# Optimization experiments

Measured on AMD Instinct MI355X. Metric: run time of the kernel, lower is better.

The kernel has to match this reference:

```python
import jax, jax.numpy as jnp
import numpy as np

H = 16      # num_heads
D = 64      # head_dim
HS = H * D  # hidden_size
B = 8
S = 1024


def setup_inputs() -> dict:
    key = jax.random.key(0)
    ks = jax.random.split(key, 12)
    scale = 1.0 / np.sqrt(HS)
    inp = {
        "v": jax.random.normal(ks[0], (B, S, HS), jnp.float32),
        "k": jax.random.normal(ks[1], (B, S, HS), jnp.float32),
        "q": jax.random.normal(ks[2], (B, S, HS), jnp.float32),
        "mask": jax.random.randint(ks[3], (B, 1, 1, S), 0, 2).astype(bool),
        "Wq": jax.random.normal(ks[4], (HS, HS), jnp.float32) * scale,
        "bq": jnp.zeros((HS,), jnp.float32),
        "Wk": jax.random.normal(ks[5], (HS, HS), jnp.float32) * scale,
        "bk": jnp.zeros((HS,), jnp.float32),
        "Wv": jax.random.normal(ks[6], (HS, HS), jnp.float32) * scale,
        "bv": jnp.zeros((HS,), jnp.float32),
        "Wo": jax.random.normal(ks[7], (HS, HS), jnp.float32) * scale,
        "bo": jnp.zeros((HS,), jnp.float32),
    }
    return inp


def _split_heads(x):
    b, s, _ = x.shape
    return x.reshape(b, s, H, D).transpose(0, 2, 1, 3)  # [B,H,S,D]


def reference(v, k, q, mask, Wq, bq, Wk, bk, Wv, bv, Wo, bo):
    # torch Linear: y = x @ W.T + b
    qh = _split_heads(q @ Wq.T + bq)
    kh = _split_heads(k @ Wk.T + bk)
    vh = _split_heads(v @ Wv.T + bv)
    scores = jnp.einsum("bhqd,bhkd->bhqk", qh, kh) / jnp.sqrt(jnp.float32(D))
    scores = jnp.where(mask, jnp.float32(-1e9), scores)
    att = jax.nn.softmax(scores, axis=-1)
    out = jnp.einsum("bhqk,bhkd->bhqd", att, vh)  # [B,H,S,D]
    out = out.transpose(0, 2, 1, 3).reshape(v.shape[0], -1, HS)
    return out @ Wo.T + bo
```

## Files before the change

kernel.cpp:

```cpp
#include <hip/hip_runtime.h>
#include <hip/hip_bf16.h>

#define HH   16
#define DD   64
#define HSZ  1024
#define BB   8
#define SS   1024
#define NTOK (BB*SS)
#define LOG2E 1.4426950408889634f
#define NCVTB 2048

typedef __attribute__((ext_vector_type(8))) short bf16x8;
typedef __attribute__((ext_vector_type(4))) float f32x4;
typedef unsigned short u16;
typedef __attribute__((ext_vector_type(4))) unsigned short u16x4;

__device__ __forceinline__ u16 bfc(float x) {
    __hip_bfloat16 h = __float2bfloat16(x);
    return *(u16*)&h;
}

__device__ __forceinline__ float exp2fast(float x) {
    return __builtin_amdgcn_exp2f(x);
}

__device__ __forceinline__ void gload16(const u16* g, u16* l) {
    __builtin_amdgcn_global_load_lds(
        (const __attribute__((address_space(1))) void*)g,
        (__attribute__((address_space(3))) void*)l, 16, 0, 0);
}

__device__ __forceinline__ void mask_scan_body(const void* mask,
                                               int* __restrict__ rmap,
                                               int* __restrict__ Larr, int b) {
    const int tid = threadIdx.x;
    const unsigned char* mball = (const unsigned char*)mask;

    __shared__ int fmt_s;
    __shared__ int wtot[4];
    __shared__ int Ls;
    if (tid == 0) fmt_s = 0;
    __syncthreads();
    int nz = 0;
    for (int i = tid; i < BB * SS; i += 256)
        if ((i & 3) && mball[i]) nz = 1;
    if (nz) fmt_s = 1;
    __syncthreads();
    const int fmt = fmt_s;

    const int base = tid * 4;
    int v[4];
#pragma unroll
    for (int e = 0; e < 4; ++e) {
        int val = fmt ? (int)mball[(size_t)b * SS + base + e]
                      : ((const int*)mask)[(size_t)b * SS + base + e];
        v[e] = (val == 0) ? 1 : 0;
    }
    int ts = v[0] + v[1] + v[2] + v[3];

    const int lane = tid & 63, wv = tid >> 6;
    int incl = ts;
#pragma unroll
    for (int d = 1; d < 64; d <<= 1) {
        int t = __shfl_up(incl, d);
        if (lane >= d) incl += t;
    }
    if (lane == 63) wtot[wv] = incl;
    __syncthreads();
    int woff = 0;
    for (int w = 0; w < wv; ++w) woff += wtot[w];
    int run = woff + incl - ts;
#pragma unroll
    for (int e = 0; e < 4; ++e) {
        if (v[e]) rmap[(size_t)b * SS + run] = base + e;
        run += v[e];
    }
    __syncthreads();
    if (tid == 0) {
        Ls = wtot[0] + wtot[1] + wtot[2] + wtot[3];
        Larr[b] = Ls;
    }
    __syncthreads();
    for (int j = Ls + tid; j < SS; j += 256) rmap[(size_t)b * SS + j] = 0;
}

__global__ __launch_bounds__(256) void cvt_scan_kernel(
        const float* __restrict__ q,  u16* __restrict__ dq,
        const float* __restrict__ k,  u16* __restrict__ dk,
        const float* __restrict__ v,  u16* __restrict__ dv,
        const float* __restrict__ w0, u16* __restrict__ dw0,
        const float* __restrict__ w1, u16* __restrict__ dw1,
        const float* __restrict__ w2, u16* __restrict__ dw2,
        const float* __restrict__ w3, u16* __restrict__ dw3,
        const void* mask, int* __restrict__ rmap, int* __restrict__ Larr) {
    if (blockIdx.x >= NCVTB) {
        mask_scan_body(mask, rmap, Larr, blockIdx.x - NCVTB);
        return;
    }
    const int NX = NTOK * HSZ / 8;
    const int NW = HSZ * HSZ / 8;
    const int ntot = 3 * NX + 4 * NW;
    int i = blockIdx.x * blockDim.x + threadIdx.x;
    const int stride = NCVTB * 256;
    for (; i < ntot; i += stride) {
        const float* s; u16* d; int j = i;
        if      (j < NX)            { s = q;  d = dq;  }
        else if ((j -= NX) < NX)    { s = k;  d = dk;  }
        else if ((j -= NX) < NX)    { s = v;  d = dv;  }
        else if ((j -= NX) < NW)    { s = w0; d = dw0; }
        else if ((j -= NW) < NW)    { s = w1; d = dw1; }
        else if ((j -= NW) < NW)    { s = w2; d = dw2; }
        else    { j -= NW;            s = w3; d = dw3; }
        f32x4 a = *(const f32x4*)&s[(size_t)j * 8];
        f32x4 b = *(const f32x4*)&s[(size_t)j * 8 + 4];
        union { bf16x8 v8; u16 u[8]; } t;
#pragma unroll
        for (int e = 0; e < 4; ++e) { t.u[e] = bfc(a[e]); t.u[4 + e] = bfc(b[e]); }
        *(bf16x8*)&d[(size_t)j * 8] = t.v8;
    }
}

template<int MODE>
__device__ __forceinline__ void proj_body(const u16* __restrict__ X,
                                          const u16* __restrict__ W,
                                          const float* __restrict__ bias,
                                          const int* __restrict__ rmap,
                                          const int* __restrict__ Larr,
                                          void* __restrict__ Yv,
                                          u16* Xs, u16* Ws) {
    const int bm = blockIdx.x;
    const int bn = blockIdx.y;
    const int tid  = threadIdx.x;
    const int wave = tid >> 6;
    const int lane = tid & 63;
    const int l15  = lane & 15;
    const int g    = lane >> 4;
    const int wr   = wave >> 1;
    const int wc   = wave & 1;

    const int b_   = bm >> 3;
    const int row0 = (bm & 7) * 128;
    if constexpr (MODE == 1 || MODE == 2) {
        const int L = Larr[b_];
        const int Lpad = ((L + 127) >> 7) << 7;
        if (row0 >= Lpad) return;
    }

    f32x4 acc[4][4] = {};

    int srow[4], scol[4], xr[4];
#pragma unroll
    for (int i = 0; i < 4; ++i) {
        const int slot = wave * 256 + i * 64 + lane;
        const int r = slot >> 3, s = slot & 7;
        srow[i] = r;
        scol[i] = (s ^ (r & 7)) * 8;
        if constexpr (MODE == 1 || MODE == 2)
            xr[i] = (b_ << 10) + rmap[(size_t)b_ * SS + row0 + r];
        else
            xr[i] = bm * 128 + r;
    }

    for (int k0 = 0; k0 < HSZ; k0 += 64) {
#pragma unroll
        for (int i = 0; i < 4; ++i) {
            gload16(&X[(size_t)xr[i] * HSZ + k0 + scol[i]], &Xs[(wave * 4 + i) * 512]);
            gload16(&W[(size_t)(bn * 128 + srow[i]) * HSZ + k0 + scol[i]],
                    &Ws[(wave * 4 + i) * 512]);
        }
        __syncthreads();

#pragma unroll
        for (int kk = 0; kk < 2; ++kk) {
            const int cw = ((kk * 4 + g) ^ (l15 & 7)) * 8;
            bf16x8 a[4], bb[4];
#pragma unroll
            for (int m = 0; m < 4; ++m)
                a[m] = *(const bf16x8*)&Xs[(size_t)(wr * 64 + m * 16 + l15) * 64 + cw];
#pragma unroll
            for (int n = 0; n < 4; ++n)
                bb[n] = *(const bf16x8*)&Ws[(size_t)(wc * 64 + n * 16 + l15) * 64 + cw];
#pragma unroll
            for (int m = 0; m < 4; ++m)
#pragma unroll
                for (int n = 0; n < 4; ++n)
                    acc[m][n] = __builtin_amdgcn_mfma_f32_16x16x32_bf16(a[m], bb[n], acc[m][n], 0, 0, 0);
        }
        __syncthreads();
    }

#pragma unroll
    for (int m = 0; m < 4; ++m) {
#pragma unroll
        for (int n = 0; n < 4; ++n) {
            const int o = bn * 128 + wc * 64 + n * 16 + l15;
            const float bvv = bias[o];
            const int h_ = o >> 6, d = o & 63;
#pragma unroll
            for (int r = 0; r < 4; ++r) {
                const int lrow = wr * 64 + m * 16 + g * 4 + r;
                float y = acc[m][n][r] + bvv;
                if constexpr (MODE == 0) {
                    const int nrow = bm * 128 + lrow;
                    int bb_ = nrow >> 10, s = nrow & 1023;
                    ((u16*)Yv)[(((size_t)bb_ * HH + h_) * SS + s) * DD + d] = bfc(y * (0.125f * LOG2E));
                } else if constexpr (MODE == 1) {
                    ((u16*)Yv)[(((size_t)b_ * HH + h_) * SS + row0 + lrow) * DD + d] = bfc(y);
                } else if constexpr (MODE == 2) {
                    ((u16*)Yv)[(((size_t)b_ * HH + h_) * DD + d) * SS + row0 + lrow] = bfc(y);
                } else {
                    const int nrow = bm * 128 + lrow;
                    ((float*)Yv)[(size_t)nrow * HSZ + o] = y;
                }
            }
        }
    }
}

__global__ __launch_bounds__(256) void proj_qkv_kernel(
        const u16* __restrict__ qbf, const u16* __restrict__ wqb,
        const float* __restrict__ bq, u16* __restrict__ Qh,
        const u16* __restrict__ kbf, const u16* __restrict__ wkb,
        const float* __restrict__ bk, u16* __restrict__ Kh,
        const u16* __restrict__ vbf, const u16* __restrict__ wvb,
        const float* __restrict__ bv, u16* __restrict__ Vt,
        const int* __restrict__ rmap, const int* __restrict__ Larr) {
    __shared__ u16 Xs[128 * 64];
    __shared__ u16 Ws[128 * 64];
    if (blockIdx.z == 0)      proj_body<0>(qbf, wqb, bq, rmap, Larr, Qh, Xs, Ws);
    else if (blockIdx.z == 1) proj_body<1>(kbf, wkb, bk, rmap, Larr, Kh, Xs, Ws);
    else                      proj_body<2>(vbf, wvb, bv, rmap, Larr, Vt, Xs, Ws);
}

__global__ __launch_bounds__(256) void proj_o_kernel(
        const u16* __restrict__ X, const u16* __restrict__ W,
        const float* __restrict__ bias, const int* __restrict__ rmap,
        const int* __restrict__ Larr, float* __restrict__ out) {
    __shared__ u16 Xs[128 * 64];
    __shared__ u16 Ws[128 * 64];
    proj_body<3>(X, W, bias, rmap, Larr, out, Xs, Ws);
}

__global__ __launch_bounds__(256, 2) void attn_kernel(const u16* __restrict__ Qh,
                                                      const u16* __restrict__ Kh,
                                                      const u16* __restrict__ Vt,
                                                      const int* __restrict__ Larr,
                                                      u16* __restrict__ ctx) {
    const int qt = blockIdx.x;
    const int h  = blockIdx.y;
    const int b  = blockIdx.z;
    const int bh = b * HH + h;

    const int tid  = threadIdx.x;
    const int wave = tid >> 6;
    const int lane = tid & 63;
    const int l15  = lane & 15;
    const int g    = lane >> 4;
    const int qw0  = qt * 256 + wave * 64;

    __shared__ u16 Pw[4][2][16][72];

    const u16* Qb = Qh + ((size_t)bh * SS + qw0) * DD;
    const u16* Kb = Kh + (size_t)bh * SS * DD;
    const u16* Vb = Vt + (size_t)bh * DD * SS;

    const int L = Larr[b];
    const int npairs = (L + 127) >> 7;

    bf16x8 qf[4][2];
#pragma unroll
    for (int qq = 0; qq < 4; ++qq)
#pragma unroll
        for (int hh = 0; hh < 2; ++hh)
            qf[qq][hh] = *(const bf16x8*)&Qb[(size_t)(qq * 16 + l15) * DD + hh * 32 + g * 8];

    f32x4 o[4][4] = {};
    float mrun[4] = { -3e38f, -3e38f, -3e38f, -3e38f };
    float lrun[4] = { 0.0f, 0.0f, 0.0f, 0.0f };

    auto loadK = [&](bf16x8 (&kbX)[8], int c0) {
#pragma unroll
        for (int kt = 0; kt < 4; ++kt)
#pragma unroll
            for (int hh = 0; hh < 2; ++hh)
                kbX[kt * 2 + hh] =
                    *(const bf16x8*)&Kb[(size_t)(c0 + kt * 16 + l15) * DD + hh * 32 + g * 8];
    };
    auto loadV = [&](bf16x8 (&vbX)[8], int c0) {
#pragma unroll
        for (int dt = 0; dt < 4; ++dt)
#pragma unroll
            for (int kh = 0; kh < 2; ++kh)
                vbX[dt * 2 + kh] =
                    *(const bf16x8*)&Vb[(size_t)(dt * 16 + l15) * SS + c0 + kh * 32 + g * 8];
    };

    auto process = [&](const bf16x8 (&kbX)[8], const bf16x8 (&vbX)[8], int c0) {
#pragma unroll
        for (int qq = 0; qq < 4; ++qq) {
            f32x4 s[4];
#pragma unroll
            for (int kt = 0; kt < 4; ++kt) {
                f32x4 a = {};
                a = __builtin_amdgcn_mfma_f32_16x16x32_bf16(kbX[kt * 2 + 0], qf[qq][0], a, 0, 0, 0);
                a = __builtin_amdgcn_mfma_f32_16x16x32_bf16(kbX[kt * 2 + 1], qf[qq][1], a, 0, 0, 0);
                s[kt] = a;
            }
            if (c0 + 64 > L) {
#pragma unroll
                for (int kt = 0; kt < 4; ++kt) {
                    const int kid = c0 + kt * 16 + g * 4;
#pragma unroll
                    for (int r = 0; r < 4; ++r)
                        s[kt][r] = (kid + r < L) ? s[kt][r] : -3e38f;
                }
            }
            float pmk[4];
#pragma unroll
            for (int kt = 0; kt < 4; ++kt)
                pmk[kt] = fmaxf(fmaxf(s[kt][0], s[kt][1]), fmaxf(s[kt][2], s[kt][3]));
            float pm = fmaxf(fmaxf(pmk[0], pmk[1]), fmaxf(pmk[2], pmk[3]));
            pm = fmaxf(pm, __shfl_xor(pm, 16));
            pm = fmaxf(pm, __shfl_xor(pm, 32));

            if (!__all(pm <= mrun[qq] + 11.5416f)) {
                float sc = exp2fast(mrun[qq] - pm);
                mrun[qq] = pm;
                lrun[qq] *= sc;
                float f0 = __shfl(sc, g * 4 + 0);
                float f1 = __shfl(sc, g * 4 + 1);
                float f2 = __shfl(sc, g * 4 + 2);
                float f3 = __shfl(sc, g * 4 + 3);
#pragma unroll
                for (int dt = 0; dt < 4; ++dt) {
                    o[qq][dt][0] *= f0; o[qq][dt][1] *= f1;
                    o[qq][dt][2] *= f2; o[qq][dt][3] *= f3;
                }
            }

            float ls = 0.0f;
#pragma unroll
            for (int kt = 0; kt < 4; ++kt) {
                union { u16x4 v; u16 u[4]; } pv;
#pragma unroll
                for (int r = 0; r < 4; ++r) {
                    float e = exp2fast(s[kt][r] - mrun[qq]);
                    ls += e;
                    pv.u[r] = bfc(e);
                }
                *(u16x4*)&Pw[wave][qq & 1][l15][kt * 16 + g * 4] = pv.v;
            }
            ls += __shfl_xor(ls, 16);
            ls += __shfl_xor(ls, 32);
            lrun[qq] += ls;

#pragma unroll
            for (int kh = 0; kh < 2; ++kh) {
                bf16x8 pa = *(const bf16x8*)&Pw[wave][qq & 1][l15][kh * 32 + g * 8];
#pragma unroll
                for (int dt = 0; dt < 4; ++dt)
                    o[qq][dt] = __builtin_amdgcn_mfma_f32_16x16x32_bf16(pa, vbX[dt * 2 + kh], o[qq][dt], 0, 0, 0);
            }
        }
    };

    bf16x8 kbA[8], kbB[8];
    loadK(kbA, 0);
    for (int t = 0; t < npairs; ++t) {
        const int cA = t * 128;
        bf16x8 vbA[8];
        loadV(vbA, cA);
        loadK(kbB, cA + 64);
        process(kbA, vbA, cA);
        bf16x8 vbB[8];
        loadV(vbB, cA + 64);
        if (t + 1 < npairs) loadK(kbA, (t + 1) * 128);
        process(kbB, vbB, cA + 64);
    }

#pragma unroll
    for (int qq = 0; qq < 4; ++qq) {
        float inv = 1.0f / lrun[qq];
        float i0 = __shfl(inv, g * 4 + 0);
        float i1 = __shfl(inv, g * 4 + 1);
        float i2 = __shfl(inv, g * 4 + 2);
        float i3 = __shfl(inv, g * 4 + 3);
#pragma unroll
        for (int dt = 0; dt < 4; ++dt) {
            const int col = h * DD + dt * 16 + l15;
            const int qr  = b * SS + qw0 + qq * 16 + g * 4;
            ctx[(size_t)(qr + 0) * HSZ + col] = bfc(o[qq][dt][0] * i0);
            ctx[(size_t)(qr + 1) * HSZ + col] = bfc(o[qq][dt][1] * i1);
            ctx[(size_t)(qr + 2) * HSZ + col] = bfc(o[qq][dt][2] * i2);
            ctx[(size_t)(qr + 3) * HSZ + col] = bfc(o[qq][dt][3] * i3);
        }
    }
}

extern "C" void kernel_launch(void* const* d_in, const int* in_sizes, int n_in,
                              void* d_out, int out_size, void* d_ws, size_t ws_size,
                              hipStream_t stream) {
    const float* v    = (const float*)d_in[0];
    const float* k    = (const float*)d_in[1];
    const float* q    = (const float*)d_in[2];
    const void*  mask = d_in[3];
    const float* Wq = (const float*)d_in[4];
    const float* bq = (const float*)d_in[5];
    const float* Wk = (const float*)d_in[6];
    const float* bk = (const float*)d_in[7];
    const float* Wv = (const float*)d_in[8];
    const float* bv = (const float*)d_in[9];
    const float* Wo = (const float*)d_in[10];
    const float* bo = (const float*)d_in[11];

    u16* qbf = (u16*)d_out;
    u16* kbf = qbf + (size_t)NTOK * HSZ;

    char* ws = (char*)d_ws;
    int*   rmap = (int*)ws;
    int*   Larr = (int*)(ws + 32768);
    u16*   wqb  = (u16*)(ws + 65536);
    u16*   wkb  = wqb + (size_t)HSZ * HSZ;
    u16*   wvb  = wkb + (size_t)HSZ * HSZ;
    u16*   wob  = wvb + (size_t)HSZ * HSZ;
    u16*   vbf  = wob + (size_t)HSZ * HSZ;
    u16*   Qh   = vbf + (size_t)NTOK * HSZ;
    u16*   Kh   = Qh + (size_t)NTOK * HSZ;
    u16*   Vt   = Kh + (size_t)NTOK * HSZ;
    u16*   ctx  = vbf;

    cvt_scan_kernel<<<NCVTB + BB, 256, 0, stream>>>(q, qbf, k, kbf, v, vbf,
                                                    Wq, wqb, Wk, wkb, Wv, wvb, Wo, wob,
                                                    mask, rmap, Larr);

    dim3 pgrid(NTOK / 128, HSZ / 128, 3);
    proj_qkv_kernel<<<pgrid, 256, 0, stream>>>(qbf, wqb, bq, Qh,
                                               kbf, wkb, bk, Kh,
                                               vbf, wvb, bv, Vt,
                                               rmap, Larr);

    dim3 agrid(SS / 256, HH, BB);
    attn_kernel<<<agrid, 256, 0, stream>>>(Qh, Kh, Vt, Larr, ctx);

    dim3 ogrid(NTOK / 128, HSZ / 128);
    proj_o_kernel<<<ogrid, 256, 0, stream>>>(ctx, wob, bo, rmap, Larr, (float*)d_out);
}
```

Before: 186.5 us.

## Stage K/V tiles through double-buffered swizzled LDS shared by all waves

Replaces per-wave direct global loads of K and V fragments with a block-wide cooperative staging of 64-key K/V chunks into double-buffered LDS, using XOR swizzling to avoid bank conflicts and async global-to-LDS loads (gload16). All four waves then read fragments from LDS, cutting redundant global/L2 traffic by 4x. It adds a __syncthreads per chunk and extra LDS usage, which may reduce occupancy or introduce barrier stalls.

New measurement: 166.0 us. 1.12x faster.

```diff
diff --git a/kernel.cpp b/kernel.cpp
--- a/kernel.cpp
+++ b/kernel.cpp
@@ -258,6 +258,8 @@
     const int g    = lane >> 4;
     const int qw0  = qt * 256 + wave * 64;
 
+    __shared__ u16 Ks[2][64 * 64];
+    __shared__ u16 Vs[2][64 * 64];
     __shared__ u16 Pw[4][2][16][72];
 
     const u16* Qb = Qh + ((size_t)bh * SS + qw0) * DD;
@@ -265,7 +267,7 @@
     const u16* Vb = Vt + (size_t)bh * DD * SS;
 
     const int L = Larr[b];
-    const int npairs = (L + 127) >> 7;
+    const int nchunks = (L + 63) >> 6;
 
     bf16x8 qf[4][2];
 #pragma unroll
@@ -278,32 +280,46 @@
     float mrun[4] = { -3e38f, -3e38f, -3e38f, -3e38f };
     float lrun[4] = { 0.0f, 0.0f, 0.0f, 0.0f };
 
-    auto loadK = [&](bf16x8 (&kbX)[8], int c0) {
+    auto stage = [&](u16* Kp, u16* Vp, int c0) {
+#pragma unroll
+        for (int i = 0; i < 2; ++i) {
+            const int slot = i * 256 + tid;
+            const int r  = slot >> 3;
+            const int cs = ((slot & 7) ^ (r & 7)) * 8;
+            u16* dstK = Kp + (size_t)(i * 256 + wave * 64) * 8;
+            u16* dstV = Vp + (size_t)(i * 256 + wave * 64) * 8;
+            gload16(&Kb[(size_t)(c0 + r) * DD + cs], dstK);
+            gload16(&Vb[(size_t)r * SS + c0 + cs],   dstV);
+        }
+    };
+    auto loadKfrag = [&](const u16* Kp, bf16x8 (&kf)[8]) {
 #pragma unroll
         for (int kt = 0; kt < 4; ++kt)
 #pragma unroll
-            for (int hh = 0; hh < 2; ++hh)
-                kbX[kt * 2 + hh] =
-                    *(const bf16x8*)&Kb[(size_t)(c0 + kt * 16 + l15) * DD + hh * 32 + g * 8];
+            for (int hh = 0; hh < 2; ++hh) {
+                const int cw = ((hh * 4 + g) ^ (l15 & 7)) * 8;
+                kf[kt * 2 + hh] = *(const bf16x8*)&Kp[(size_t)(kt * 16 + l15) * 64 + cw];
+            }
     };
-    auto loadV = [&](bf16x8 (&vbX)[8], int c0) {
+    auto loadVfrag = [&](const u16* Vp, bf16x8 (&vf)[8]) {
 #pragma unroll
         for (int dt = 0; dt < 4; ++dt)
 #pragma unroll
-            for (int kh = 0; kh < 2; ++kh)
-                vbX[dt * 2 + kh] =
-                    *(const bf16x8*)&Vb[(size_t)(dt * 16 + l15) * SS + c0 + kh * 32 + g * 8];
+            for (int kh = 0; kh < 2; ++kh) {
+                const int cw = ((kh * 4 + g) ^ (l15 & 7)) * 8;
+                vf[dt * 2 + kh] = *(const bf16x8*)&Vp[(size_t)(dt * 16 + l15) * 64 + cw];
+            }
     };
 
-    auto process = [&](const bf16x8 (&kbX)[8], const bf16x8 (&vbX)[8], int c0) {
+    auto process = [&](const bf16x8 (&kf)[8], const bf16x8 (&vf)[8], int c0) {
 #pragma unroll
         for (int qq = 0; qq < 4; ++qq) {
             f32x4 s[4];
 #pragma unroll
             for (int kt = 0; kt < 4; ++kt) {
                 f32x4 a = {};
-                a = __builtin_amdgcn_mfma_f32_16x16x32_bf16(kbX[kt * 2 + 0], qf[qq][0], a, 0, 0, 0);
-                a = __builtin_amdgcn_mfma_f32_16x16x32_bf16(kbX[kt * 2 + 1], qf[qq][1], a, 0, 0, 0);
+                a = __builtin_amdgcn_mfma_f32_16x16x32_bf16(kf[kt * 2 + 0], qf[qq][0], a, 0, 0, 0);
+                a = __builtin_amdgcn_mfma_f32_16x16x32_bf16(kf[kt * 2 + 1], qf[qq][1], a, 0, 0, 0);
                 s[kt] = a;
             }
             if (c0 + 64 > L) {
@@ -359,23 +375,21 @@
                 bf16x8 pa = *(const bf16x8*)&Pw[wave][qq & 1][l15][kh * 32 + g * 8];
 #pragma unroll
                 for (int dt = 0; dt < 4; ++dt)
-                    o[qq][dt] = __builtin_amdgcn_mfma_f32_16x16x32_bf16(pa, vbX[dt * 2 + kh], o[qq][dt], 0, 0, 0);
+                    o[qq][dt] = __builtin_amdgcn_mfma_f32_16x16x32_bf16(pa, vf[dt * 2 + kh], o[qq][dt], 0, 0, 0);
             }
         }
     };
 
-    bf16x8 kbA[8], kbB[8];
-    loadK(kbA, 0);
-    for (int t = 0; t < npairs; ++t) {
-        const int cA = t * 128;
-        bf16x8 vbA[8];
-        loadV(vbA, cA);
-        loadK(kbB, cA + 64);
-        process(kbA, vbA, cA);
-        bf16x8 vbB[8];
-        loadV(vbB, cA + 64);
-        if (t + 1 < npairs) loadK(kbA, (t + 1) * 128);
-        process(kbB, vbB, cA + 64);
+    stage(&Ks[0][0], &Vs[0][0], 0);
+    __syncthreads();
+    for (int c = 0; c < nchunks; ++c) {
+        const int p = c & 1;
+        if (c + 1 < nchunks) stage(&Ks[p ^ 1][0], &Vs[p ^ 1][0], (c + 1) * 64);
+        bf16x8 kf[8], vf[8];
+        loadKfrag(&Ks[p][0], kf);
+        loadVfrag(&Vs[p][0], vf);
+        process(kf, vf, c * 64);
+        __syncthreads();
     }
 
 #pragma unroll
```
